# Performance work log

Hardware: AMD Instinct MI355X
Metric: run time of the kernel (lower is better)

Reference implementation:

```python
import jax, jax.numpy as jnp
import numpy as np

N = 50000        # total nodes (disjoint batch of graphs)
E = 800000       # total edges
F_IN = 8         # node feature dim
S = 6            # edge feature dim
H = 20           # ECC kernel-network hidden size (hidden_states)
N_OUT = 20       # ECC output channels (n_out=hidden_states)
G = 32           # GCN channels
D1 = 16          # first dense
N_GRAPHS = 512   # graphs in batch


def setup_inputs() -> dict:
    key = jax.random.key(0)
    ks = jax.random.split(key, 24)
    r = lambda k, sh, s: jax.random.normal(k, sh, dtype=jnp.float32) * s
    return {
        "x": r(ks[0], (N, F_IN), 1.0),
        "e": r(ks[1], (E, S), 1.0),
        "edge_index": jax.random.randint(ks[2], (2, E), 0, N, dtype=jnp.int32),
        "seg": jnp.sort(jax.random.randint(ks[3], (N,), 0, N_GRAPHS, dtype=jnp.int32)),
        # ECC kernel network: S -> H -> H -> F_IN*N_OUT
        "ecc_w1": r(ks[4], (S, H), 0.4), "ecc_b1": jnp.zeros((H,), jnp.float32),
        "ecc_w2": r(ks[5], (H, H), 0.2), "ecc_b2": jnp.zeros((H,), jnp.float32),
        "ecc_w3": r(ks[6], (H, F_IN * N_OUT), 0.2), "ecc_b3": jnp.zeros((F_IN * N_OUT,), jnp.float32),
        "ecc_root": r(ks[7], (F_IN, N_OUT), 0.3), "ecc_b": jnp.zeros((N_OUT,), jnp.float32),
        "gcn1_w": r(ks[8], (N_OUT, G), 0.2), "gcn1_b": jnp.zeros((G,), jnp.float32),
        "gcn2_w": r(ks[9], (G, G), 0.2), "gcn2_b": jnp.zeros((G,), jnp.float32),
        "d1_w": r(ks[10], (G, D1), 0.2), "d1_b": jnp.zeros((D1,), jnp.float32),
        "d2_w": r(ks[11], (D1, 1), 0.2), "d2_b": jnp.zeros((1,), jnp.float32),
    }


def reference(x, e, edge_index, seg,
              ecc_w1, ecc_b1, ecc_w2, ecc_b2, ecc_w3, ecc_b3, ecc_root, ecc_b,
              gcn1_w, gcn1_b, gcn2_w, gcn2_b, d1_w, d1_b, d2_w, d2_b):
    row, col = edge_index[0], edge_index[1]  # message col -> row

    # --- ECCConv: per-edge MLP produces an [F_IN, N_OUT] filter per edge ---
    h = jax.nn.relu(e @ ecc_w1 + ecc_b1)
    h = jax.nn.relu(h @ ecc_w2 + ecc_b2)
    w_edge = (h @ ecc_w3 + ecc_b3).reshape(E, F_IN, N_OUT)   # [E, F_in, F_out]
    msg = jnp.einsum('ef,efo->eo', x[col], w_edge)            # per-edge message
    agg = jax.ops.segment_sum(msg, row, num_segments=N)
    x1 = jax.nn.relu(agg + x @ ecc_root + ecc_b)              # root + bias + relu

    # --- GCN normalization from the edge list (A + I, symmetric norm) ---
    deg = jax.ops.segment_sum(jnp.ones((E,), x.dtype), row, num_segments=N) + 1.0
    dinv = jax.lax.rsqrt(deg)
    edge_norm = (dinv[row] * dinv[col])[:, None]
    self_norm = (dinv * dinv)[:, None]

    def gcn(hin, W, b):
        hw = hin @ W
        nmsg = jax.ops.segment_sum(edge_norm * hw[col], row, num_segments=N)
        return jax.nn.relu(nmsg + self_norm * hw + b)

    x2 = gcn(x1, gcn1_w, gcn1_b)
    x3 = gcn(x2, gcn2_w, gcn2_b)

    # --- GlobalSumPool over graph ids, then MLP head ---
    pooled = jax.ops.segment_sum(x3, seg, num_segments=N_GRAPHS)  # [n_graphs, G]
    out = (pooled @ d1_w + d1_b) @ d2_w + d2_b                    # [n_graphs, 1]
    return out
```

## Files before the change

### kernel.cpp

```cpp
#include <hip/hip_runtime.h>

#define S_DIM   6
#define H_DIM   20
#define F_INN   8
#define N_OUTC  20
#define G_DIM   32
#define D1_DIM  16
#define NGRAPH  512
#define CAP     32

typedef short short8 __attribute__((ext_vector_type(8)));
typedef float floatx4 __attribute__((ext_vector_type(4)));

__device__ __forceinline__ unsigned short f2bf(float f) {
    unsigned u = __float_as_uint(f);
    return (unsigned short)((u + 0x8000u) >> 16);
}
__device__ __forceinline__ float bf2f(unsigned short s) {
    return __uint_as_float(((unsigned)s) << 16);
}

__global__ __launch_bounds__(256) void prep_kernel(
    const float* __restrict__ w3, const float* __restrict__ b3,
    unsigned short* __restrict__ B3f)
{
    int idx = blockIdx.x * 256 + threadIdx.x;
    if (idx >= 6144) return;
    int jj   = idx & 7;
    int n    = (idx >> 3) & 15;
    int quad = (idx >> 7) & 3;
    int nt   = (idx >> 9) & 1;
    int s    = idx >> 10;
    int K = 32 * s + quad * 8 + jj;
    int o = n + 16 * nt;
    float v = 0.0f;
    if (o < N_OUTC) {
        if (K < 160)      v = w3[(K >> 3) * 160 + (K & 7) * N_OUTC + o];
        else if (K < 168) v = b3[(K - 160) * N_OUTC + o];
    }
    B3f[idx] = f2bf(v);
}

__global__ __launch_bounds__(256) void loc_kernel(
    const int* __restrict__ ei, int E, int* __restrict__ cnt,
    int* __restrict__ loc)
{
    int i = blockIdx.x * 256 + threadIdx.x;
    if (i >= E) return;
    loc[i] = atomicAdd(&cnt[ei[i]], 1);
}

__global__ __launch_bounds__(256) void scanA_kernel(
    const int* __restrict__ deg, int N, int* __restrict__ bsum)
{
    int i = blockIdx.x * 256 + threadIdx.x;
    int v = (i < N) ? deg[i] : 0;
#pragma unroll
    for (int d = 1; d < 64; d <<= 1) v += __shfl_down(v, d, 64);
    __shared__ int ws[4];
    int wid = threadIdx.x >> 6;
    if ((threadIdx.x & 63) == 0) ws[wid] = v;
    __syncthreads();
    if (threadIdx.x == 0) bsum[blockIdx.x] = ws[0] + ws[1] + ws[2] + ws[3];
}

__global__ __launch_bounds__(256) void scanC_kernel(
    const int* __restrict__ deg, int N, const int* __restrict__ bsum, int nbl,
    int E, int* __restrict__ rowptr, float* __restrict__ dinv)
{
    __shared__ int ws[4];
    __shared__ int sboff;
    int t = threadIdx.x;
    {
        int v = (t < nbl && t < blockIdx.x) ? bsum[t] : 0;
#pragma unroll
        for (int d = 1; d < 64; d <<= 1) v += __shfl_down(v, d, 64);
        int wid = t >> 6;
        if ((t & 63) == 0) ws[wid] = v;
        __syncthreads();
        if (t == 0) sboff = ws[0] + ws[1] + ws[2] + ws[3];
        __syncthreads();
    }

    int i = blockIdx.x * 256 + t;
    int d0 = (i < N) ? deg[i] : 0;
    int v = d0;
#pragma unroll
    for (int d = 1; d < 64; d <<= 1) {
        int u = __shfl_up(v, d, 64);
        if ((t & 63) >= d) v += u;
    }
    __shared__ int ws2[4];
    int wid = t >> 6;
    if ((t & 63) == 63) ws2[wid] = v;
    __syncthreads();
    int woff = 0;
    for (int w = 0; w < wid; ++w) woff += ws2[w];
    if (i < N) {
        rowptr[i] = sboff + woff + v - d0;
        dinv[i] = rsqrtf((float)d0 + 1.0f);
    }
    if (blockIdx.x == 0 && t == 0) rowptr[N] = E;
}

__global__ __launch_bounds__(256) void build_kernel(
    const int* __restrict__ ei, int E, const float* __restrict__ e,
    const int* __restrict__ rowptr, const int* __restrict__ loc,
    int4* __restrict__ e_sorted)
{
    int i = blockIdx.x * 256 + threadIdx.x;
    if (i >= E) return;
    int r = ei[i];
    int c = ei[E + i];
    int p = rowptr[r] + loc[i];

    const float2* ep = (const float2*)&e[(size_t)i * S_DIM];
    float2 e0 = ep[0], e1 = ep[1], e2 = ep[2];

    int4 rec;
    rec.x = c;
    rec.y = (int)f2bf(e0.x) | ((int)f2bf(e0.y) << 16);
    rec.z = (int)f2bf(e1.x) | ((int)f2bf(e1.y) << 16);
    rec.w = (int)f2bf(e2.x) | ((int)f2bf(e2.y) << 16);
    e_sorted[p] = rec;
}

__global__ __launch_bounds__(256) void ecc_mfma_kernel(
    const int4* __restrict__ e_sorted, const float* __restrict__ x,
    const int* __restrict__ rowptr, int N, int E,
    const unsigned short* __restrict__ B3f,
    const float* __restrict__ w1, const float* __restrict__ b1,
    const float* __restrict__ w2, const float* __restrict__ b2,
    const float* __restrict__ root, const float* __restrict__ eb,
    const float* __restrict__ g1w,
    float* __restrict__ agg, int* __restrict__ col_sorted,
    unsigned short* __restrict__ hws1)
{
    __shared__ char smem[20480];
    __shared__ float x1buf[CAP * N_OUTC];
    __shared__ int rbounds[2];
    unsigned short (*h2b)[N_OUTC] = (unsigned short (*)[N_OUTC])smem;
    unsigned short (*xb)[F_INN]   = (unsigned short (*)[F_INN])(smem + 10240);
    float* lmsg = (float*)smem;

    int t = threadIdx.x;
    int j0 = blockIdx.x * 256;
    int jend = min(j0 + 256, E);
    int j = j0 + t;

    if (t < 2) {
        int s = (t == 0) ? j0 : (jend - 1);
        int lo = 0, hi = N - 1;
        while (lo < hi) {
            int m = (lo + hi + 1) >> 1;
            if (rowptr[m] <= s) lo = m; else hi = m - 1;
        }
        rbounds[t] = lo;
    }

    if (j < E) {
        int4 rec = e_sorted[j];
        int c = rec.x;
        col_sorted[j] = c;
        float ef[S_DIM] = {
            bf2f((unsigned short)(rec.y & 0xffff)),
            bf2f((unsigned short)((unsigned)rec.y >> 16)),
            bf2f((unsigned short)(rec.z & 0xffff)),
            bf2f((unsigned short)((unsigned)rec.z >> 16)),
            bf2f((unsigned short)(rec.w & 0xffff)),
            bf2f((unsigned short)((unsigned)rec.w >> 16))
        };

        float h1[H_DIM];
#pragma unroll
        for (int jj = 0; jj < H_DIM; ++jj) {
            float a = b1[jj];
#pragma unroll
            for (int s = 0; s < S_DIM; ++s) a = fmaf(ef[s], w1[s * H_DIM + jj], a);
            h1[jj] = fmaxf(a, 0.0f);
        }

        float h2[H_DIM];
#pragma unroll
        for (int jj = 0; jj < H_DIM; ++jj) {
            float a = b2[jj];
#pragma unroll
            for (int k = 0; k < H_DIM; ++k) a = fmaf(h1[k], w2[k * H_DIM + jj], a);
            h2[jj] = fmaxf(a, 0.0f);
        }

        const float4* xp = (const float4*)&x[(size_t)c * F_INN];
        float4 xa = xp[0], xb4 = xp[1];
        float xf[F_INN] = {xa.x, xa.y, xa.z, xa.w, xb4.x, xb4.y, xb4.z, xb4.w};

#pragma unroll
        for (int o = 0; o < N_OUTC; ++o) h2b[t][o] = f2bf(h2[o]);
#pragma unroll
        for (int f = 0; f < F_INN; ++f) xb[t][f] = f2bf(xf[f]);
    } else {
#pragma unroll
        for (int o = 0; o < N_OUTC; ++o) h2b[t][o] = 0;
#pragma unroll
        for (int f = 0; f < F_INN; ++f) xb[t][f] = 0;
    }
    __syncthreads();

    int lane = t & 63;
    int quad = lane >> 4;
    int n = lane & 15;
    const short8* Bg = (const short8*)B3f;
    short8 Bf[12];
#pragma unroll
    for (int s = 0; s < 6; ++s)
#pragma unroll
        for (int nt = 0; nt < 2; ++nt)
            Bf[s * 2 + nt] = Bg[((s * 2 + nt) * 4 + quad) * 16 + n];

    int w = t >> 6;
    floatx4 acc0s[4], acc1s[4];
#pragma unroll
    for (int T = 0; T < 4; ++T) {
        int base = w * 64 + T * 16;
        int m = base + n;

        const short8 xv8 = *(const short8*)&xb[m][0];
        float xfl[F_INN];
#pragma unroll
        for (int jj = 0; jj < F_INN; ++jj) xfl[jj] = bf2f((unsigned short)xv8[jj]);

        floatx4 acc0 = {0.f, 0.f, 0.f, 0.f};
        floatx4 acc1 = {0.f, 0.f, 0.f, 0.f};
#pragma unroll
        for (int s = 0; s < 6; ++s) {
            short8 A = {0, 0, 0, 0, 0, 0, 0, 0};
            if (s < 5) {
                float h = bf2f(h2b[m][4 * s + quad]);
#pragma unroll
                for (int jj = 0; jj < F_INN; ++jj)
                    A[jj] = (short)f2bf(h * xfl[jj]);
            } else if (quad == 0) {
                A = xv8;
            }
            acc0 = __builtin_amdgcn_mfma_f32_16x16x32_bf16(A, Bf[s * 2 + 0], acc0, 0, 0, 0);
            acc1 = __builtin_amdgcn_mfma_f32_16x16x32_bf16(A, Bf[s * 2 + 1], acc1, 0, 0, 0);
        }
        acc0s[T] = acc0;
        acc1s[T] = acc1;
    }
    __syncthreads();

#pragma unroll
    for (int T = 0; T < 4; ++T) {
        int base = w * 64 + T * 16;
#pragma unroll
        for (int r = 0; r < 4; ++r) {
            int row = base + quad * 4 + r;
            lmsg[row * N_OUTC + n] = acc0s[T][r];
            if (n < 4) lmsg[row * N_OUTC + 16 + n] = acc1s[T][r];
        }
    }
    __syncthreads();

    int r0 = rbounds[0], r1 = rbounds[1];
    int nrows = r1 - r0 + 1;
    int work = nrows * 5;
    for (int ww = t; ww < work; ww += 256) {
        int idx = ww / 5;
        int q = ww - idx * 5;
        int row = r0 + idx;
        int a0 = rowptr[row], a1 = rowptr[row + 1];
        int s0 = max(a0, j0), s1 = min(a1, jend);
        float ac0 = 0.f, ac1 = 0.f, ac2 = 0.f, ac3 = 0.f;
        for (int s = s0; s < s1; ++s) {
            const float4 v = *(const float4*)&lmsg[(s - j0) * N_OUTC + q * 4];
            ac0 += v.x; ac1 += v.y; ac2 += v.z; ac3 += v.w;
        }
        bool owned = (a0 >= j0 && a1 <= jend);
        if (owned && idx < CAP) {
            const float4* xp = (const float4*)&x[(size_t)row * F_INN];
            float4 xa = xp[0], xb4 = xp[1];
            float rx[F_INN] = {xa.x, xa.y, xa.z, xa.w, xb4.x, xb4.y, xb4.z, xb4.w};
            float av[4] = {ac0, ac1, ac2, ac3};
#pragma unroll
            for (int u = 0; u < 4; ++u) {
                int oc = q * 4 + u;
                float a = av[u] + eb[oc];
#pragma unroll
                for (int f = 0; f < F_INN; ++f)
                    a = fmaf(rx[f], root[f * N_OUTC + oc], a);
                x1buf[idx * N_OUTC + oc] = fmaxf(a, 0.0f);
            }
        } else {
            float* dst = &agg[(size_t)row * N_OUTC + q * 4];
            if (owned) {
                *(float4*)dst = make_float4(ac0, ac1, ac2, ac3);
            } else {
                unsafeAtomicAdd(dst + 0, ac0);
                unsafeAtomicAdd(dst + 1, ac1);
                unsafeAtomicAdd(dst + 2, ac2);
                unsafeAtomicAdd(dst + 3, ac3);
            }
        }
    }
    __syncthreads();

    int fast = min(nrows, CAP);
    int work2 = fast * 8;
    for (int ww = t; ww < work2; ww += 256) {
        int idx = ww >> 3;
        int qc = ww & 7;
        int row = r0 + idx;
        int a0 = rowptr[row], a1 = rowptr[row + 1];
        if (!(a0 >= j0 && a1 <= jend)) continue;
        float di = rsqrtf((float)(a1 - a0) + 1.0f);
        float m0 = 0.f, m1 = 0.f, m2 = 0.f, m3 = 0.f;
        const float* xr = &x1buf[idx * N_OUTC];
#pragma unroll
        for (int o = 0; o < N_OUTC; ++o) {
            float xv = xr[o];
            const float4 g = *(const float4*)&g1w[o * G_DIM + qc * 4];
            m0 = fmaf(xv, g.x, m0); m1 = fmaf(xv, g.y, m1);
            m2 = fmaf(xv, g.z, m2); m3 = fmaf(xv, g.w, m3);
        }
        unsigned lo32 = (unsigned)f2bf(m0 * di) | ((unsigned)f2bf(m1 * di) << 16);
        unsigned hi32 = (unsigned)f2bf(m2 * di) | ((unsigned)f2bf(m3 * di) << 16);
        *(uint2*)&hws1[(size_t)row * G_DIM + qc * 4] = make_uint2(lo32, hi32);
    }
}

__global__ __launch_bounds__(256) void cleanup_kernel(
    const float* __restrict__ agg, const float* __restrict__ x,
    const int* __restrict__ rowptr, int N,
    const float* __restrict__ root, const float* __restrict__ eb,
    const float* __restrict__ g1w,
    unsigned short* __restrict__ hws1)
{
    int n = blockIdx.x * 256 + threadIdx.x;
    if (n >= N) return;
    int a0 = rowptr[n], a1 = rowptr[n + 1];
    bool contained = (a1 > a0) ? ((a0 >> 8) == ((a1 - 1) >> 8))
                               : ((a0 & 255) != 0);
    if (contained) {
        int target = (a0 >> 8) << 8;
        int lo = 0, hi = N - 1;
        while (lo < hi) {
            int m = (lo + hi + 1) >> 1;
            if (rowptr[m] <= target) lo = m; else hi = m - 1;
        }
        if (n - lo < CAP) return;
    }

    const float4* xp = (const float4*)&x[(size_t)n * F_INN];
    float4 xa = xp[0], xb = xp[1];
    float xf[F_INN] = {xa.x, xa.y, xa.z, xa.w, xb.x, xb.y, xb.z, xb.w};

    float x1[N_OUTC];
#pragma unroll
    for (int o = 0; o < N_OUTC; ++o) {
        float a = agg[(size_t)n * N_OUTC + o] + eb[o];
#pragma unroll
        for (int f = 0; f < F_INN; ++f) a = fmaf(xf[f], root[f * N_OUTC + o], a);
        x1[o] = fmaxf(a, 0.0f);
    }

    float di = rsqrtf((float)(a1 - a0) + 1.0f);
#pragma unroll
    for (int q = 0; q < 4; ++q) {
        short8 o8;
#pragma unroll
        for (int u = 0; u < 8; ++u) {
            int g = q * 8 + u;
            float a = 0.0f;
#pragma unroll
            for (int o = 0; o < N_OUTC; ++o) a = fmaf(x1[o], g1w[o * G_DIM + g], a);
            o8[u] = (short)f2bf(a * di);
        }
        *(short8*)&hws1[(size_t)n * G_DIM + q * 8] = o8;
    }
}

template<bool DO_MATMUL>
__global__ __launch_bounds__(256) void gcn_gather_kernel(
    const unsigned short* __restrict__ hws, const int* __restrict__ rowptr,
    const int* __restrict__ col_sorted, const float* __restrict__ dinv, int N,
    const float* __restrict__ bias, const float* __restrict__ w2,
    unsigned short* __restrict__ outbuf)
{
    __shared__ float x2s[64][33];
    __shared__ float w2s[G_DIM * G_DIM];

    int t = threadIdx.x;
    int nl = t >> 2;
    int q = t & 3;
    int n = blockIdx.x * 64 + nl;

    if (DO_MATMUL) {
        ((float4*)w2s)[t] = ((const float4*)w2)[t];
    }

    float xo[8];
    float di = 0.0f;
    if (n < N) {
        di = dinv[n];
        int j0 = rowptr[n], j1 = rowptr[n + 1];
        short8 sv = *(const short8*)&hws[(size_t)n * G_DIM + q * 8];
        float s[8];
#pragma unroll
        for (int k = 0; k < 8; ++k) s[k] = bf2f((unsigned short)sv[k]);
#pragma unroll 2
        for (int j = j0; j < j1; ++j) {
            int c = col_sorted[j];
            short8 v = *(const short8*)&hws[(size_t)c * G_DIM + q * 8];
#pragma unroll
            for (int k = 0; k < 8; ++k) s[k] += bf2f((unsigned short)v[k]);
        }
#pragma unroll
        for (int k = 0; k < 8; ++k)
            xo[k] = fmaxf(fmaf(di, s[k], bias[q * 8 + k]), 0.0f);
    } else {
#pragma unroll
        for (int k = 0; k < 8; ++k) xo[k] = 0.0f;
    }

    if (DO_MATMUL) {
#pragma unroll
        for (int k = 0; k < 8; ++k) x2s[nl][q * 8 + k] = xo[k];
        __syncthreads();
        if (n < N) {
            float a[8];
#pragma unroll
            for (int k = 0; k < 8; ++k) a[k] = 0.0f;
#pragma unroll
            for (int g = 0; g < G_DIM; ++g) {
                float xv = x2s[nl][g];
#pragma unroll
                for (int k = 0; k < 8; ++k)
                    a[k] = fmaf(xv, w2s[g * G_DIM + q * 8 + k], a[k]);
            }
            short8 o8;
#pragma unroll
            for (int k = 0; k < 8; ++k) o8[k] = (short)f2bf(a[k] * di);
            *(short8*)&outbuf[(size_t)n * G_DIM + q * 8] = o8;
        }
    } else {
        if (n < N) {
            short8 o8;
#pragma unroll
            for (int k = 0; k < 8; ++k) o8[k] = (short)f2bf(xo[k]);
            *(short8*)&outbuf[(size_t)n * G_DIM + q * 8] = o8;
        }
    }
}

__global__ __launch_bounds__(256) void pool_head_kernel(
    const unsigned short* __restrict__ x3, const int* __restrict__ seg, int N,
    const float* __restrict__ d1w, const float* __restrict__ d1b,
    const float* __restrict__ d2w, const float* __restrict__ d2b,
    float* __restrict__ out)
{
    __shared__ float red[8][G_DIM];
    __shared__ float pvec[G_DIM];
    __shared__ int bounds[2];
    int g = blockIdx.x;
    int t = threadIdx.x;
    if (t < 2) {
        int target = g + t;
        int lo = 0, hi = N;
        while (lo < hi) {
            int m = (lo + hi) >> 1;
            if (seg[m] < target) lo = m + 1; else hi = m;
        }
        bounds[t] = lo;
    }
    __syncthreads();
    int n0 = bounds[0], n1 = bounds[1];
    int ch = t & (G_DIM - 1);
    int slice = t >> 5;
    float a = 0.0f;
    for (int n = n0 + slice; n < n1; n += 8)
        a += bf2f(x3[(size_t)n * G_DIM + ch]);
    red[slice][ch] = a;
    __syncthreads();
    if (slice == 0) {
        float s = red[0][ch];
#pragma unroll
        for (int k = 1; k < 8; ++k) s += red[k][ch];
        pvec[ch] = s;
    }
    __syncthreads();
    if (t < 64) {
        float acc = 0.0f;
        if (t < D1_DIM) {
            float tj = d1b[t];
#pragma unroll
            for (int gg = 0; gg < G_DIM; ++gg)
                tj = fmaf(pvec[gg], d1w[gg * D1_DIM + t], tj);
            acc = tj * d2w[t];
        }
#pragma unroll
        for (int d = 1; d < D1_DIM; d <<= 1) acc += __shfl_down(acc, d, 64);
        if (t == 0) out[g] = acc + d2b[0];
    }
}

extern "C" void kernel_launch(void* const* d_in, const int* in_sizes, int n_in,
                              void* d_out, int out_size, void* d_ws, size_t ws_size,
                              hipStream_t stream)
{
    const float* x    = (const float*)d_in[0];
    const float* e    = (const float*)d_in[1];
    const int*   ei   = (const int*)d_in[2];
    const int*   seg  = (const int*)d_in[3];
    const float* w1   = (const float*)d_in[4];
    const float* b1   = (const float*)d_in[5];
    const float* w2   = (const float*)d_in[6];
    const float* b2   = (const float*)d_in[7];
    const float* w3   = (const float*)d_in[8];
    const float* b3   = (const float*)d_in[9];
    const float* root = (const float*)d_in[10];
    const float* eb   = (const float*)d_in[11];
    const float* g1w  = (const float*)d_in[12];
    const float* g1b  = (const float*)d_in[13];
    const float* g2w  = (const float*)d_in[14];
    const float* g2b  = (const float*)d_in[15];
    const float* d1w  = (const float*)d_in[16];
    const float* d1b  = (const float*)d_in[17];
    const float* d2w  = (const float*)d_in[18];
    const float* d2b  = (const float*)d_in[19];

    const int N = in_sizes[3];
    const int E = in_sizes[1] / S_DIM;
    float* out = (float*)d_out;

    const int nbl = (N + 255) / 256;
    const int ebl = (E + 255) / 256;

    char* ws = (char*)d_ws;
    size_t off = 0;
    auto alloc = [&](size_t elems) -> char* {
        char* p = ws + off;
        off += ((elems * 4 + 15) & ~(size_t)15);
        return p;
    };
    int*   cnt        = (int*)  alloc(N);
    float* agg        = (float*)alloc((size_t)N * N_OUTC);
    size_t zero_bytes = off;
    int*   rowptr     = (int*)  alloc(N + 1);
    int*   bsum       = (int*)  alloc(nbl);
    float* dinv       = (float*)alloc(N);
    int*   loc        = (int*)  alloc(E);
    int*   col_sorted = (int*)  alloc(E);
    unsigned short* B3f = (unsigned short*)alloc(6144 / 2);
    int4*  e_sorted   = (int4*) alloc((size_t)E * 4);
    unsigned short* hws1 = (unsigned short*)alloc((size_t)N * G_DIM / 2);
    unsigned short* hws2 = (unsigned short*)alloc((size_t)N * G_DIM / 2);
    unsigned short* x3   = (unsigned short*)alloc((size_t)N * G_DIM / 2);
    (void)ws_size;

    hipMemsetAsync(d_ws, 0, zero_bytes, stream);

    prep_kernel<<<24, 256, 0, stream>>>(w3, b3, B3f);
    loc_kernel<<<ebl, 256, 0, stream>>>(ei, E, cnt, loc);
    scanA_kernel<<<nbl, 256, 0, stream>>>(cnt, N, bsum);
    scanC_kernel<<<nbl, 256, 0, stream>>>(cnt, N, bsum, nbl, E, rowptr, dinv);
    build_kernel<<<ebl, 256, 0, stream>>>(ei, E, e, rowptr, loc, e_sorted);
    ecc_mfma_kernel<<<ebl, 256, 0, stream>>>(e_sorted, x, rowptr, N, E, B3f,
                                             w1, b1, w2, b2, root, eb, g1w,
                                             agg, col_sorted, hws1);
    cleanup_kernel<<<nbl, 256, 0, stream>>>(agg, x, rowptr, N, root, eb, g1w, hws1);
    gcn_gather_kernel<true><<<(N + 63) / 64, 256, 0, stream>>>(
        hws1, rowptr, col_sorted, dinv, N, g1b, g2w, hws2);
    gcn_gather_kernel<false><<<(N + 63) / 64, 256, 0, stream>>>(
        hws2, rowptr, col_sorted, dinv, N, g2b, nullptr, x3);
    pool_head_kernel<<<NGRAPH, 256, 0, stream>>>(x3, seg, N, d1w, d1b, d2w, d2b, out);
}
```

Before: 264.4 us.

## Fuse global sum pooling into final GCN gather and merge prep into loc kernel

Merges the B3 weight-prep kernel into loc_kernel and recomputes dinv from rowptr instead of storing it. The final GCN gather now pools straight into a per-graph buffer through LDS atomics, falling back to global atomics, instead of writing x3 and rescanning it. A small per-graph head kernel replaces the pool_head kernel. Neighbour column indices for each block are staged in shared memory. Together these cut kernel launches and the x3 round trip, at the cost of atomics, extra LDS use and non-deterministic summation order.

```diff
diff --git a/kernel.cpp b/kernel.cpp
--- a/kernel.cpp
+++ b/kernel.cpp
@@ -8,6 +8,7 @@
 #define D1_DIM  16
 #define NGRAPH  512
 #define CAP     32
+#define COLCAP  2048
 
 typedef short short8 __attribute__((ext_vector_type(8)));
 typedef float floatx4 __attribute__((ext_vector_type(4)));
@@ -20,32 +21,28 @@
     return __uint_as_float(((unsigned)s) << 16);
 }
 
-__global__ __launch_bounds__(256) void prep_kernel(
+__global__ __launch_bounds__(256) void loc_kernel(
+    const int* __restrict__ ei, int E, int* __restrict__ cnt,
+    int* __restrict__ loc,
     const float* __restrict__ w3, const float* __restrict__ b3,
     unsigned short* __restrict__ B3f)
 {
-    int idx = blockIdx.x * 256 + threadIdx.x;
-    if (idx >= 6144) return;
-    int jj   = idx & 7;
-    int n    = (idx >> 3) & 15;
-    int quad = (idx >> 7) & 3;
-    int nt   = (idx >> 9) & 1;
-    int s    = idx >> 10;
-    int K = 32 * s + quad * 8 + jj;
-    int o = n + 16 * nt;
-    float v = 0.0f;
-    if (o < N_OUTC) {
-        if (K < 160)      v = w3[(K >> 3) * 160 + (K & 7) * N_OUTC + o];
-        else if (K < 168) v = b3[(K - 160) * N_OUTC + o];
-    }
-    B3f[idx] = f2bf(v);
-}
-
-__global__ __launch_bounds__(256) void loc_kernel(
-    const int* __restrict__ ei, int E, int* __restrict__ cnt,
-    int* __restrict__ loc)
-{
     int i = blockIdx.x * 256 + threadIdx.x;
+    if (i < 6144) {
+        int jj   = i & 7;
+        int n    = (i >> 3) & 15;
+        int quad = (i >> 7) & 3;
+        int nt   = (i >> 9) & 1;
+        int s    = i >> 10;
+        int K = 32 * s + quad * 8 + jj;
+        int o = n + 16 * nt;
+        float v = 0.0f;
+        if (o < N_OUTC) {
+            if (K < 160)      v = w3[(K >> 3) * 160 + (K & 7) * N_OUTC + o];
+            else if (K < 168) v = b3[(K - 160) * N_OUTC + o];
+        }
+        B3f[i] = f2bf(v);
+    }
     if (i >= E) return;
     loc[i] = atomicAdd(&cnt[ei[i]], 1);
 }
@@ -66,7 +63,7 @@
 
 __global__ __launch_bounds__(256) void scanC_kernel(
     const int* __restrict__ deg, int N, const int* __restrict__ bsum, int nbl,
-    int E, int* __restrict__ rowptr, float* __restrict__ dinv)
+    int E, int* __restrict__ rowptr)
 {
     __shared__ int ws[4];
     __shared__ int sboff;
@@ -96,10 +93,7 @@
     __syncthreads();
     int woff = 0;
     for (int w = 0; w < wid; ++w) woff += ws2[w];
-    if (i < N) {
-        rowptr[i] = sboff + woff + v - d0;
-        dinv[i] = rsqrtf((float)d0 + 1.0f);
-    }
+    if (i < N) rowptr[i] = sboff + woff + v - d0;
     if (blockIdx.x == 0 && t == 0) rowptr[N] = E;
 }
 
@@ -379,37 +373,59 @@
     }
 }
 
-template<bool DO_MATMUL>
+template<bool DO_MATMUL, bool DO_POOL>
 __global__ __launch_bounds__(256) void gcn_gather_kernel(
     const unsigned short* __restrict__ hws, const int* __restrict__ rowptr,
-    const int* __restrict__ col_sorted, const float* __restrict__ dinv, int N,
+    const int* __restrict__ col_sorted, const int* __restrict__ seg, int N,
     const float* __restrict__ bias, const float* __restrict__ w2,
-    unsigned short* __restrict__ outbuf)
-{
-    __shared__ float x2s[64][33];
-    __shared__ float w2s[G_DIM * G_DIM];
+    unsigned short* __restrict__ outbuf, float* __restrict__ pooled)
+{
+    __shared__ int colbuf[COLCAP];
+    __shared__ int binfo[2];
+    __shared__ float x2s[DO_MATMUL ? 64 * 33 : 1];
+    __shared__ float w2s[DO_MATMUL ? G_DIM * G_DIM : 1];
+    __shared__ float pbuf[DO_POOL ? 64 * G_DIM : 1];
+    __shared__ int ginfo[2];
 
     int t = threadIdx.x;
+    int n0 = blockIdx.x * 64;
+    int nend = min(n0 + 64, N);
+
+    if (t == 0) { binfo[0] = rowptr[n0]; binfo[1] = rowptr[nend]; }
+    if (DO_MATMUL) ((float4*)w2s)[t] = ((const float4*)w2)[t];
+    if (DO_POOL) {
+        if (t == 0) {
+            int gmin = seg[n0];
+            int gmax = seg[nend - 1];
+            ginfo[0] = gmin;
+            ginfo[1] = (gmax - gmin < 64) ? 1 : 0;
+        }
+        for (int k = t; k < 64 * G_DIM; k += 256) pbuf[k] = 0.0f;
+    }
+    __syncthreads();
+
+    int jb0 = binfo[0];
+    int cap = min(binfo[1] - jb0, COLCAP);
+    for (int k = t; k < cap; k += 256) colbuf[k] = col_sorted[jb0 + k];
+    __syncthreads();
+
     int nl = t >> 2;
     int q = t & 3;
-    int n = blockIdx.x * 64 + nl;
-
-    if (DO_MATMUL) {
-        ((float4*)w2s)[t] = ((const float4*)w2)[t];
-    }
+    int n = n0 + nl;
 
     float xo[8];
     float di = 0.0f;
     if (n < N) {
-        di = dinv[n];
         int j0 = rowptr[n], j1 = rowptr[n + 1];
+        di = rsqrtf((float)(j1 - j0) + 1.0f);
         short8 sv = *(const short8*)&hws[(size_t)n * G_DIM + q * 8];
         float s[8];
 #pragma unroll
         for (int k = 0; k < 8; ++k) s[k] = bf2f((unsigned short)sv[k]);
 #pragma unroll 2
         for (int j = j0; j < j1; ++j) {
-            int c = col_sorted[j];
+            int idx = j - jb0;
+            int c = (idx < COLCAP) ? colbuf[idx] : col_sorted[j];
             short8 v = *(const short8*)&hws[(size_t)c * G_DIM + q * 8];
 #pragma unroll
             for (int k = 0; k < 8; ++k) s[k] += bf2f((unsigned short)v[k]);
@@ -424,7 +440,7 @@
 
     if (DO_MATMUL) {
 #pragma unroll
-        for (int k = 0; k < 8; ++k) x2s[nl][q * 8 + k] = xo[k];
+        for (int k = 0; k < 8; ++k) x2s[nl * 33 + q * 8 + k] = xo[k];
         __syncthreads();
         if (n < N) {
             float a[8];
@@ -432,7 +448,7 @@
             for (int k = 0; k < 8; ++k) a[k] = 0.0f;
 #pragma unroll
             for (int g = 0; g < G_DIM; ++g) {
-                float xv = x2s[nl][g];
+                float xv = x2s[nl * 33 + g];
 #pragma unroll
                 for (int k = 0; k < 8; ++k)
                     a[k] = fmaf(xv, w2s[g * G_DIM + q * 8 + k], a[k]);
@@ -442,6 +458,30 @@
             for (int k = 0; k < 8; ++k) o8[k] = (short)f2bf(a[k] * di);
             *(short8*)&outbuf[(size_t)n * G_DIM + q * 8] = o8;
         }
+    } else if (DO_POOL) {
+        int gmin = ginfo[0];
+        int use_lds = ginfo[1];
+        if (n < N) {
+            int sg = seg[n];
+            if (use_lds) {
+                float* base = &pbuf[(sg - gmin) * G_DIM + q * 8];
+#pragma unroll
+                for (int k = 0; k < 8; ++k) atomicAdd(&base[k], xo[k]);
+            } else {
+#pragma unroll
+                for (int k = 0; k < 8; ++k)
+                    unsafeAtomicAdd(&pooled[(size_t)sg * G_DIM + q * 8 + k], xo[k]);
+            }
+        }
+        __syncthreads();
+        if (use_lds) {
+            for (int k = t; k < 64 * G_DIM; k += 256) {
+                float v = pbuf[k];
+                int g = gmin + (k >> 5);
+                if (v != 0.0f && g < NGRAPH)
+                    unsafeAtomicAdd(&pooled[(size_t)g * G_DIM + (k & 31)], v);
+            }
+        }
     } else {
         if (n < N) {
             short8 o8;
@@ -452,55 +492,28 @@
     }
 }
 
-__global__ __launch_bounds__(256) void pool_head_kernel(
-    const unsigned short* __restrict__ x3, const int* __restrict__ seg, int N,
+__global__ __launch_bounds__(256) void head_kernel(
+    const float* __restrict__ pooled,
     const float* __restrict__ d1w, const float* __restrict__ d1b,
     const float* __restrict__ d2w, const float* __restrict__ d2b,
     float* __restrict__ out)
 {
-    __shared__ float red[8][G_DIM];
-    __shared__ float pvec[G_DIM];
-    __shared__ int bounds[2];
-    int g = blockIdx.x;
-    int t = threadIdx.x;
-    if (t < 2) {
-        int target = g + t;
-        int lo = 0, hi = N;
-        while (lo < hi) {
-            int m = (lo + hi) >> 1;
-            if (seg[m] < target) lo = m + 1; else hi = m;
-        }
-        bounds[t] = lo;
-    }
-    __syncthreads();
-    int n0 = bounds[0], n1 = bounds[1];
-    int ch = t & (G_DIM - 1);
-    int slice = t >> 5;
-    float a = 0.0f;
-    for (int n = n0 + slice; n < n1; n += 8)
-        a += bf2f(x3[(size_t)n * G_DIM + ch]);
-    red[slice][ch] = a;
-    __syncthreads();
-    if (slice == 0) {
-        float s = red[0][ch];
-#pragma unroll
-        for (int k = 1; k < 8; ++k) s += red[k][ch];
-        pvec[ch] = s;
-    }
-    __syncthreads();
-    if (t < 64) {
-        float acc = 0.0f;
-        if (t < D1_DIM) {
-            float tj = d1b[t];
-#pragma unroll
-            for (int gg = 0; gg < G_DIM; ++gg)
-                tj = fmaf(pvec[gg], d1w[gg * D1_DIM + t], tj);
-            acc = tj * d2w[t];
-        }
-#pragma unroll
-        for (int d = 1; d < D1_DIM; d <<= 1) acc += __shfl_down(acc, d, 64);
-        if (t == 0) out[g] = acc + d2b[0];
-    }
+    int i = blockIdx.x * 256 + threadIdx.x;
+    if (i >= NGRAPH) return;
+
+    float p[G_DIM];
+#pragma unroll
+    for (int g = 0; g < G_DIM; ++g) p[g] = pooled[i * G_DIM + g];
+
+    float acc = d2b[0];
+#pragma unroll
+    for (int j = 0; j < D1_DIM; ++j) {
+        float tj = d1b[j];
+#pragma unroll
+        for (int g = 0; g < G_DIM; ++g) tj = fmaf(p[g], d1w[g * D1_DIM + j], tj);
+        acc = fmaf(tj, d2w[j], acc);
+    }
+    out[i] = acc;
 }
 
 extern "C" void kernel_launch(void* const* d_in, const int* in_sizes, int n_in,
@@ -544,33 +557,31 @@
     };
     int*   cnt        = (int*)  alloc(N);
     float* agg        = (float*)alloc((size_t)N * N_OUTC);
+    float* pooled     = (float*)alloc(NGRAPH * G_DIM);
     size_t zero_bytes = off;
     int*   rowptr     = (int*)  alloc(N + 1);
     int*   bsum       = (int*)  alloc(nbl);
-    float* dinv       = (float*)alloc(N);
     int*   loc        = (int*)  alloc(E);
     int*   col_sorted = (int*)  alloc(E);
     unsigned short* B3f = (unsigned short*)alloc(6144 / 2);
     int4*  e_sorted   = (int4*) alloc((size_t)E * 4);
     unsigned short* hws1 = (unsigned short*)alloc((size_t)N * G_DIM / 2);
     unsigned short* hws2 = (unsigned short*)alloc((size_t)N * G_DIM / 2);
-    unsigned short* x3   = (unsigned short*)alloc((size_t)N * G_DIM / 2);
     (void)ws_size;
 
     hipMemsetAsync(d_ws, 0, zero_bytes, stream);
 
-    prep_kernel<<<24, 256, 0, stream>>>(w3, b3, B3f);
-    loc_kernel<<<ebl, 256, 0, stream>>>(ei, E, cnt, loc);
+    loc_kernel<<<ebl, 256, 0, stream>>>(ei, E, cnt, loc, w3, b3, B3f);
     scanA_kernel<<<nbl, 256, 0, stream>>>(cnt, N, bsum);
-    scanC_kernel<<<nbl, 256, 0, stream>>>(cnt, N, bsum, nbl, E, rowptr, dinv);
+    scanC_kernel<<<nbl, 256, 0, stream>>>(cnt, N, bsum, nbl, E, rowptr);
     build_kernel<<<ebl, 256, 0, stream>>>(ei, E, e, rowptr, loc, e_sorted);
     ecc_mfma_kernel<<<ebl, 256, 0, stream>>>(e_sorted, x, rowptr, N, E, B3f,
                                              w1, b1, w2, b2, root, eb, g1w,
                                              agg, col_sorted, hws1);
     cleanup_kernel<<<nbl, 256, 0, stream>>>(agg, x, rowptr, N, root, eb, g1w, hws1);
-    gcn_gather_kernel<true><<<(N + 63) / 64, 256, 0, stream>>>(
-        hws1, rowptr, col_sorted, dinv, N, g1b, g2w, hws2);
-    gcn_gather_kernel<false><<<(N + 63) / 64, 256, 0, stream>>>(
-        hws2, rowptr, col_sorted, dinv, N, g2b, nullptr, x3);
-    pool_head_kernel<<<NGRAPH, 256, 0, stream>>>(x3, seg, N, d1w, d1b, d2w, d2b, out);
-}
+    gcn_gather_kernel<true, false><<<(N + 63) / 64, 256, 0, stream>>>(
+        hws1, rowptr, col_sorted, seg, N, g1b, g2w, hws2, nullptr);
+    gcn_gather_kernel<false, true><<<(N + 63) / 64, 256, 0, stream>>>(
+        hws2, rowptr, col_sorted, seg, N, g2b, nullptr, nullptr, pooled);
+    head_kernel<<<(NGRAPH + 255) / 256, 256, 0, stream>>>(pooled, d1w, d1b, d2w, d2b, out);
+}
```

After: 267.1 us. Within noise of the previous version (+1.0%).
